# Kernel tuning notes

Measured on AMD Instinct MI355X. Metric: run time of the kernel, lower is better.

Reference implementation:

```python
import jax, jax.numpy as jnp
import numpy as np

VOCAB = 100000
DIM = 300
SEQ = 200
BATCH = 1024


def setup_inputs() -> dict:
    key = jax.random.key(0)
    ks = jax.random.split(key, 7)
    tokens = jax.random.randint(ks[0], (SEQ, BATCH), 0, VOCAB, dtype=jnp.int32)
    static_lut = jax.random.normal(ks[1], (VOCAB, DIM), dtype=jnp.float32)
    # lut = pretrained vectors + N(0, 0.01) noise
    lut = static_lut + 0.01 * jax.random.normal(ks[2], (VOCAB, DIM), dtype=jnp.float32)
    W1 = jax.random.normal(ks[3], (600, 600), dtype=jnp.float32) / np.sqrt(600.0)
    b1 = jnp.zeros((600,), dtype=jnp.float32)
    W2 = jax.random.normal(ks[4], (1, 600), dtype=jnp.float32) / np.sqrt(600.0)
    b2 = jnp.zeros((1,), dtype=jnp.float32)
    return {"tokens": tokens, "lut": lut, "static_lut": static_lut,
            "W1": W1, "b1": b1, "W2": W2, "b2": b2}


def _first_occurrence_mask(tokens):
    # tokens: [S, B]. mask[i, b] = 1 iff tokens[i, b] is the first occurrence
    # of that token value in column b (emulates per-column set() dedup).
    S = tokens.shape[0]
    eq = tokens[:, None, :] == tokens[None, :, :]          # [S, S, B]
    first_idx = jnp.argmax(eq, axis=1)                      # [S, B] first j with same token
    return (first_idx == jnp.arange(S, dtype=first_idx.dtype)[:, None])


def reference(tokens, lut, static_lut, W1, b1, W2, b2):
    mask = _first_occurrence_mask(tokens).astype(lut.dtype)  # [S, B]
    # dedup embedding-bag sums over unique tokens per column
    e_learn = jnp.einsum('sbd,sb->bd', lut[tokens], mask)          # [B, 300]
    e_static = jnp.einsum('sbd,sb->bd', static_lut[tokens], mask)  # [B, 300]
    hidden = jnp.concatenate([e_learn, e_static], axis=-1)         # [B, 600]
    h = jax.nn.relu(hidden @ W1.T + b1)                            # [B, 600]
    out = h @ W2.T + b2                                            # [B, 1]
    return out[:, 0]                                               # [B]
```

## Files before the change

### kernel.cpp

```cpp
#include <hip/hip_runtime.h>
#include <limits.h>

#define SEQ   200
#define BATCH 1024
#define DIM   300
#define HID   600
#define VOCAB 100000

#define NQ    4

#define BW    4
#define JCH   12
#define JPER  (HID / JCH)

#define HIDDEN_ELEMS (BATCH * HID)
#define HIDDEN_BYTES ((size_t)HIDDEN_ELEMS * 4)

__global__ __launch_bounds__(256) void embed_sort_kernel(
    const int* __restrict__ tokens,
    const float* __restrict__ lut,
    const float* __restrict__ slut,
    float* __restrict__ hid4) {
  const int b   = blockIdx.x;
  const int q   = blockIdx.y;
  const int tid = threadIdx.x;

  __shared__ int toks[SEQ];
  __shared__ int stok[256];
  __shared__ int nk_sh;

  for (int s = tid; s < SEQ; s += 256) toks[s] = tokens[s * BATCH + b];
  if (tid == 0) nk_sh = 0;
  __syncthreads();

  int my = INT_MAX;
  if (tid < SEQ) {
    const int t = toks[tid];
    bool k = true;
    for (int p = 0; p < tid; ++p) {
      if (toks[p] == t) { k = false; break; }
    }
    if (k) my = t;
  }
  stok[tid] = my;
  if (my != INT_MAX) atomicAdd(&nk_sh, 1);
  __syncthreads();

  for (int k = 2; k <= 256; k <<= 1) {
    for (int j = k >> 1; j > 0; j >>= 1) {
      const int ixj = tid ^ j;
      if (ixj > tid) {
        const int a = stok[tid];
        const int c = stok[ixj];
        const bool up = ((tid & k) == 0);
        if ((a > c) == up) { stok[tid] = c; stok[ixj] = a; }
      }
      __syncthreads();
    }
  }

  const int nk = nk_sh;
  const int i0 = (q * nk) / NQ;
  const int i1 = ((q + 1) * nk) / NQ;

  const int tab_i = tid / 75;
  const int slot  = tid % 75;
  if (tab_i < 2) {
    const float* __restrict__ tab = tab_i ? slut : lut;
    float4 a = make_float4(0.f, 0.f, 0.f, 0.f);
#pragma unroll 4
    for (int i = i0; i < i1; ++i) {
      const float4 v = ((const float4*)(tab + (size_t)stok[i] * DIM))[slot];
      a.x += v.x; a.y += v.y; a.z += v.z; a.w += v.w;
    }
    float* dst = hid4 + ((size_t)q * BATCH + b) * HID + tab_i * DIM;
    ((float4*)dst)[slot] = a;
  }
}

__global__ __launch_bounds__(256) void combine_kernel(
    const float* __restrict__ hid4, float* __restrict__ hidden) {
  const int i = blockIdx.x * 256 + threadIdx.x;
  const int n4 = HIDDEN_ELEMS / 4;
  if (i < n4) {
    const float4* p = (const float4*)hid4;
    const float4 a = p[i];
    const float4 b = p[i + n4];
    const float4 c = p[i + 2 * n4];
    const float4 d = p[i + 3 * n4];
    float4 s;
    s.x = (a.x + b.x) + (c.x + d.x);
    s.y = (a.y + b.y) + (c.y + d.y);
    s.z = (a.z + b.z) + (c.z + d.z);
    s.w = (a.w + b.w) + (c.w + d.w);
    ((float4*)hidden)[i] = s;
  }
}

__global__ __launch_bounds__(256) void out_init_kernel(
    float* __restrict__ out, const float* __restrict__ b2) {
  const int i = blockIdx.x * 256 + threadIdx.x;
  if (i < BATCH) out[i] = b2[0];
}

template <int CTRL>
__device__ __forceinline__ float dpp_add(float x) {
  const int y = __builtin_amdgcn_update_dpp(
      0, __float_as_int(x), CTRL, 0xf, 0xf, true);
  return x + __int_as_float(y);
}

__device__ __forceinline__ float wave_sum(float h) {
  h = dpp_add<0x111>(h);
  h = dpp_add<0x112>(h);
  h = dpp_add<0x114>(h);
  h = dpp_add<0x118>(h);
  h = dpp_add<0x142>(h);
  h = dpp_add<0x143>(h);
  return h;
}

__global__ __launch_bounds__(256) void mlp_kernel(
    const float* __restrict__ hidden,
    const float* __restrict__ W1,
    const float* __restrict__ b1,
    const float* __restrict__ W2,
    float* __restrict__ out) {
  const int wave = threadIdx.x >> 6;
  const int lane = threadIdx.x & 63;
  const int b0   = (blockIdx.x * 4 + wave) * BW;
  const int j0   = blockIdx.y * JPER;

  float a[BW][10];
#pragma unroll
  for (int bb = 0; bb < BW; ++bb) {
    const float* __restrict__ hb = hidden + (size_t)(b0 + bb) * HID;
#pragma unroll
    for (int i = 0; i < 9; ++i) a[bb][i] = hb[lane + 64 * i];
    a[bb][9] = (lane < 24) ? hb[lane + 576] : 0.f;
  }

  float acc[BW] = {0.f, 0.f, 0.f, 0.f};

#pragma unroll 2
  for (int jj = 0; jj < JPER; ++jj) {
    const int j = j0 + jj;
    const float* __restrict__ wr = W1 + (size_t)j * HID;
    float d0 = 0.f, d1 = 0.f, d2 = 0.f, d3 = 0.f;
#pragma unroll
    for (int i = 0; i < 9; ++i) {
      const float w = wr[lane + 64 * i];
      d0 += a[0][i] * w;
      d1 += a[1][i] * w;
      d2 += a[2][i] * w;
      d3 += a[3][i] * w;
    }
    {
      const float w = (lane < 24) ? wr[lane + 576] : 0.f;
      d0 += a[0][9] * w;
      d1 += a[1][9] * w;
      d2 += a[2][9] * w;
      d3 += a[3][9] * w;
    }
    d0 = wave_sum(d0); d1 = wave_sum(d1);
    d2 = wave_sum(d2); d3 = wave_sum(d3);
    const float b1j = b1[j];
    const float w2j = W2[j];
    acc[0] += fmaxf(d0 + b1j, 0.f) * w2j;
    acc[1] += fmaxf(d1 + b1j, 0.f) * w2j;
    acc[2] += fmaxf(d2 + b1j, 0.f) * w2j;
    acc[3] += fmaxf(d3 + b1j, 0.f) * w2j;
  }

  if (lane == 63) {
#pragma unroll
    for (int bb = 0; bb < BW; ++bb) atomicAdd(&out[b0 + bb], acc[bb]);
  }
}

extern "C" void kernel_launch(void* const* d_in, const int* in_sizes, int n_in,
                              void* d_out, int out_size, void* d_ws, size_t ws_size,
                              hipStream_t stream) {
  const int*   tokens = (const int*)  d_in[0];
  const float* lut    = (const float*)d_in[1];
  const float* slut   = (const float*)d_in[2];
  const float* W1     = (const float*)d_in[3];
  const float* b1     = (const float*)d_in[4];
  const float* W2     = (const float*)d_in[5];
  const float* b2     = (const float*)d_in[6];
  float* out = (float*)d_out;

  float* hid4   = (float*)d_ws;
  float* hidden = (float*)((char*)d_ws + 4 * HIDDEN_BYTES);

  out_init_kernel<<<(BATCH + 255) / 256, 256, 0, stream>>>(out, b2);
  embed_sort_kernel<<<dim3(BATCH, NQ), 256, 0, stream>>>(
      tokens, lut, slut, hid4);
  combine_kernel<<<(HIDDEN_ELEMS / 4 + 255) / 256, 256, 0, stream>>>(
      hid4, hidden);
  mlp_kernel<<<dim3(BATCH / (4 * BW), JCH), 256, 0, stream>>>(
      hidden, W1, b1, W2, out);
}
```

Measured before the change: 129.0 us.

## Split dedup sort into separate kernel to avoid redundant per-quarter sorting

Moves the per-column dedup and bitonic sort into its own kernel that writes sorted unique tokens and counts to workspace. The gather kernel then reads these and sums embedding rows using 192-thread blocks with deeper unrolling. This removes the fourfold redundant sorting done by each quarter block, at the cost of an extra launch and a small global-memory round-trip.

```diff
diff --git a/kernel.cpp b/kernel.cpp
--- a/kernel.cpp
+++ b/kernel.cpp
@@ -16,13 +16,17 @@
 #define HIDDEN_ELEMS (BATCH * HID)
 #define HIDDEN_BYTES ((size_t)HIDDEN_ELEMS * 4)
 
-__global__ __launch_bounds__(256) void embed_sort_kernel(
+#define SORT_BYTES  ((size_t)BATCH * 256 * 4)
+#define NK_BYTES    ((size_t)BATCH * 4)
+#define OFF_NK      SORT_BYTES
+#define OFF_HID4    (SORT_BYTES + 65536)
+#define OFF_HIDDEN  (OFF_HID4 + 4 * HIDDEN_BYTES)
+
+__global__ __launch_bounds__(256) void sort_kernel(
     const int* __restrict__ tokens,
-    const float* __restrict__ lut,
-    const float* __restrict__ slut,
-    float* __restrict__ hid4) {
+    int* __restrict__ sorted_g,
+    int* __restrict__ nk_g) {
   const int b   = blockIdx.x;
-  const int q   = blockIdx.y;
   const int tid = threadIdx.x;
 
   __shared__ int toks[SEQ];
@@ -59,7 +63,21 @@
     }
   }
 
-  const int nk = nk_sh;
+  sorted_g[b * 256 + tid] = stok[tid];
+  if (tid == 0) nk_g[b] = nk_sh;
+}
+
+__global__ __launch_bounds__(192) void embed_gather_kernel(
+    const int* __restrict__ sorted_g,
+    const int* __restrict__ nk_g,
+    const float* __restrict__ lut,
+    const float* __restrict__ slut,
+    float* __restrict__ hid4) {
+  const int b   = blockIdx.x;
+  const int q   = blockIdx.y;
+  const int tid = threadIdx.x;
+
+  const int nk = nk_g[b];
   const int i0 = (q * nk) / NQ;
   const int i1 = ((q + 1) * nk) / NQ;
 
@@ -67,10 +85,11 @@
   const int slot  = tid % 75;
   if (tab_i < 2) {
     const float* __restrict__ tab = tab_i ? slut : lut;
+    const int* __restrict__ rows = sorted_g + b * 256;
     float4 a = make_float4(0.f, 0.f, 0.f, 0.f);
-#pragma unroll 4
+#pragma unroll 8
     for (int i = i0; i < i1; ++i) {
-      const float4 v = ((const float4*)(tab + (size_t)stok[i] * DIM))[slot];
+      const float4 v = ((const float4*)(tab + (size_t)rows[i] * DIM))[slot];
       a.x += v.x; a.y += v.y; a.z += v.z; a.w += v.w;
     }
     float* dst = hid4 + ((size_t)q * BATCH + b) * HID + tab_i * DIM;
@@ -190,12 +209,15 @@
   const float* b2     = (const float*)d_in[6];
   float* out = (float*)d_out;
 
-  float* hid4   = (float*)d_ws;
-  float* hidden = (float*)((char*)d_ws + 4 * HIDDEN_BYTES);
+  int*   sorted_g = (int*)d_ws;
+  int*   nk_g     = (int*)((char*)d_ws + OFF_NK);
+  float* hid4     = (float*)((char*)d_ws + OFF_HID4);
+  float* hidden   = (float*)((char*)d_ws + OFF_HIDDEN);
 
   out_init_kernel<<<(BATCH + 255) / 256, 256, 0, stream>>>(out, b2);
-  embed_sort_kernel<<<dim3(BATCH, NQ), 256, 0, stream>>>(
-      tokens, lut, slut, hid4);
+  sort_kernel<<<BATCH, 256, 0, stream>>>(tokens, sorted_g, nk_g);
+  embed_gather_kernel<<<dim3(BATCH, NQ), 192, 0, stream>>>(
+      sorted_g, nk_g, lut, slut, hid4);
   combine_kernel<<<(HIDDEN_ELEMS / 4 + 255) / 256, 256, 0, stream>>>(
       hid4, hidden);
   mlp_kernel<<<dim3(BATCH / (4 * BW), JCH), 256, 0, stream>>>(
```

Measured after the change: 131.4 us. About the same (+1.9%).
